# Performance work log

Hardware: AMD Instinct MI355X
Metric: run time of the kernel (lower is better)

The kernel has to match this reference:

```python
import jax, jax.numpy as jnp
import numpy as np

N, E, R, L = 20000, 160000, 3, 2
IN, HID, H, OUT = 64, 128, 16, 1
FH = HID // H   # per-head dim = 8
HD2 = HID // 2  # MLP bottleneck = 64


def setup_inputs() -> dict:
    key = jax.random.key(0)
    ks = iter(jax.random.split(key, 40))
    def w(*shape):
        return jax.random.normal(next(ks), shape, jnp.float32) * 0.05
    inp = dict(
        inputs=jax.random.normal(next(ks), (N, IN), jnp.float32),
        src=jax.random.randint(next(ks), (R, E), 0, N, dtype=jnp.int32),
        dst=jax.random.randint(next(ks), (R, E), 0, N, dtype=jnp.int32),
        e1_W=w(IN, HID), e1_b=jnp.zeros(HID), e_g=jnp.ones(HID), e_bt=jnp.zeros(HID),
        e2_W=w(HID, HID), e2_b=jnp.zeros(HID),
        gat_W=w(L, R, HID, HID), gat_al=w(L, R, H, FH), gat_ar=w(L, R, H, FH),
        gat_b=jnp.zeros((L, R, HID)),
        attn_p=w(L, R, HID),
        m1_W=w(L, HID, HD2), m1_b=jnp.zeros((L, HD2)), m_g=jnp.ones((L, HD2)), m_bt=jnp.zeros((L, HD2)),
        m2_W=w(L, HD2, HID), m2_b=jnp.zeros((L, HID)),
        d1_W=w(HID, HD2), d1_b=jnp.zeros(HD2), d_g=jnp.ones(HD2), d_bt=jnp.zeros(HD2),
        d2_W=w(HD2, OUT), d2_b=jnp.zeros(OUT),
    )
    return inp


def _bn(x, g, b):
    # BatchNorm1d, training mode: biased batch statistics, eps=1e-5
    mu = x.mean(0)
    var = jnp.mean((x - mu) ** 2, 0)
    return g * (x - mu) * jax.lax.rsqrt(var + 1e-5) + b


def _mlp(x, W1, b1, g, bt, W2, b2, skip=False):
    h = jax.nn.relu(_bn(x @ W1 + b1, g, bt))
    o = h @ W2 + b2
    return o + h if skip else o


def _gat(x, W, al, ar, b, src, dst):
    # single-relation DGL GATConv (feat_drop=attn_drop=0, neg_slope=0.2, bias)
    z = (x @ W).reshape(N, H, FH)                 # [N,H,FH]
    el = (z * al).sum(-1)                          # [N,H]
    er = (z * ar).sum(-1)                          # [N,H]
    e = jax.nn.leaky_relu(el[src] + er[dst], 0.2)  # [E,H]
    m = jax.ops.segment_max(e, dst, num_segments=N)
    m = jnp.where(jnp.isfinite(m), m, 0.0)
    ex = jnp.exp(e - m[dst])
    s = jax.ops.segment_sum(ex, dst, num_segments=N)
    alpha = ex / s[dst]                            # edge softmax over in-edges
    out = jax.ops.segment_sum(alpha[:, :, None] * z[src], dst, num_segments=N)
    return out.reshape(N, HID) + b                 # flatten heads + bias


def reference(inputs, src, dst, e1_W, e1_b, e_g, e_bt, e2_W, e2_b,
              gat_W, gat_al, gat_ar, gat_b, attn_p,
              m1_W, m1_b, m_g, m_bt, m2_W, m2_b,
              d1_W, d1_b, d_g, d_bt, d2_W, d2_b):
    h = _mlp(inputs, e1_W, e1_b, e_g, e_bt, e2_W, e2_b, skip=True)  # embed, skip
    gat_v = jax.vmap(_gat, in_axes=(None, 0, 0, 0, 0, 0, 0))        # over relations
    for l in range(L):
        stacked = gat_v(h, gat_W[l], gat_al[l], gat_ar[l], gat_b[l], src, dst)  # [R,N,HID]
        w = jax.nn.softmax(attn_p[l], axis=0)        # per-dim softmax over relations [R,HID]
        v = jnp.einsum('rnf,rf->nf', stacked, w)     # attn-weighted relation agg
        h = _mlp(v, m1_W[l], m1_b[l], m_g[l], m_bt[l], m2_W[l], m2_b[l]) + h
    return _mlp(h, d1_W, d1_b, d_g, d_bt, d2_W, d2_b)
```

## Files before the change

### kernel.cpp

```cpp
#include <hip/hip_runtime.h>
#include <math.h>

constexpr int kN   = 20000;
constexpr int kE   = 160000;
constexpr int kR   = 3;
constexpr int kL   = 2;
constexpr int kIN  = 64;
constexpr int kHID = 128;
constexpr int kH   = 16;
constexpr int kFH  = 8;
constexpr int kHD2 = 64;

typedef __bf16 bf16x8 __attribute__((ext_vector_type(8)));
typedef float  f32x4  __attribute__((ext_vector_type(4)));

__device__ __forceinline__ bf16x8 ldfrag(const __bf16* p) {
  return __builtin_bit_cast(bf16x8, *(const uint4*)p);
}
__device__ __forceinline__ f32x4 MF(bf16x8 a, bf16x8 b, f32x4 c) {
  return __builtin_amdgcn_mfma_f32_16x16x32_bf16(a, b, c, 0, 0, 0);
}

__device__ __forceinline__ void splitrow(const float* __restrict__ rowbase, int koff,
                                         bool bn, const float* scS, const float* shS,
                                         bf16x8& hi, bf16x8& lo) {
  float4 xa = *(const float4*)(rowbase + koff);
  float4 xb = *(const float4*)(rowbase + koff + 4);
  float x[8] = {xa.x, xa.y, xa.z, xa.w, xb.x, xb.y, xb.z, xb.w};
  union { __bf16 b[8]; bf16x8 v; } uh, ul;
#pragma unroll
  for (int e = 0; e < 8; e++) {
    float y = x[e];
    if (bn) y = fmaxf(fmaf(y, scS[koff + e], shS[koff + e]), 0.f);
    __bf16 hb = (__bf16)y;
    uh.b[e] = hb;
    ul.b[e] = (__bf16)(y - (float)hb);
  }
  hi = uh.v; lo = ul.v;
}

__global__ __launch_bounds__(256) void mgemm_kernel(
    const float* __restrict__ A, const __bf16* __restrict__ WT,
    const float* __restrict__ bias, const float* __restrict__ resf, int resmode,
    const float* __restrict__ bnstat, const float* __restrict__ bng,
    const float* __restrict__ bnbt, float invn,
    float* __restrict__ statS,
    float* __restrict__ Cf, __bf16* __restrict__ Chi,
    const float* __restrict__ alb, const float* __restrict__ arb,
    float* __restrict__ elout,
    int n, int k, int m, long wstride, long cstride) {
  __shared__ __bf16 Bh[64][136];
  __shared__ __bf16 Bl[64][136];
  __shared__ float scS[128], shS[128];
  const int t  = threadIdx.x;
  const int w  = t >> 6;
  const int l  = t & 63;
  const int lr = l & 15;
  const int lg = l >> 4;
  const int rb = blockIdx.x * 128 + w * 32;
  const int c0 = blockIdx.y * 64;
  const __bf16* Whi = WT + (size_t)blockIdx.z * wstride;
  const __bf16* Wlo = Whi + (size_t)k * m;
  if (Chi) Chi += (size_t)blockIdx.z * cstride;
  const float* al = alb ? alb + blockIdx.z * kHID : nullptr;
  const float* ar = arb ? arb + blockIdx.z * kHID : nullptr;
  float* elo = elout ? elout + blockIdx.z * 32 : nullptr;

  const bool bn = bnstat != nullptr;
  if (bn && t < k) {
    float mu  = bnstat[t] * invn;
    float var = bnstat[k + t] * invn - mu * mu;
    float s = bng[t] * rsqrtf(var + 1e-5f);
    scS[t] = s; shS[t] = bnbt[t] - mu * s;
  }
  const int kseg = k >> 3;
  for (int idx = t; idx < 64 * kseg; idx += 256) {
    int col = idx / kseg, seg = idx - col * kseg;
    *(uint4*)&Bh[col][seg * 8] = *(const uint4*)&Whi[(size_t)(c0 + col) * k + seg * 8];
    *(uint4*)&Bl[col][seg * 8] = *(const uint4*)&Wlo[(size_t)(c0 + col) * k + seg * 8];
  }
  __syncthreads();

  int r0 = rb + lr;      if (r0 > n - 1) r0 = n - 1;
  int r1 = rb + 16 + lr; if (r1 > n - 1) r1 = n - 1;
  f32x4 acc[2][4] = {};

  for (int ks = 0; ks < (k >> 5); ks++) {
    const int koff = ks * 32 + lg * 8;
    bf16x8 a0h, a0l, a1h, a1l;
    splitrow(&A[(size_t)r0 * k], koff, bn, scS, shS, a0h, a0l);
    splitrow(&A[(size_t)r1 * k], koff, bn, scS, shS, a1h, a1l);
#pragma unroll
    for (int j = 0; j < 4; j++) {
      bf16x8 bh = ldfrag(&Bh[j * 16 + lr][koff]);
      bf16x8 bl = ldfrag(&Bl[j * 16 + lr][koff]);
      acc[0][j] = MF(a0h, bh, acc[0][j]);
      acc[0][j] = MF(a0l, bh, acc[0][j]);
      acc[0][j] = MF(a0h, bl, acc[0][j]);
      acc[1][j] = MF(a1h, bh, acc[1][j]);
      acc[1][j] = MF(a1l, bh, acc[1][j]);
      acc[1][j] = MF(a1h, bl, acc[1][j]);
    }
  }

  float s[4] = {}, s2[4] = {};
#pragma unroll
  for (int i = 0; i < 2; i++) {
#pragma unroll
    for (int q = 0; q < 4; q++) {
      int row = rb + i * 16 + lg * 4 + q;
      bool ok = row < n;
#pragma unroll
      for (int j = 0; j < 4; j++) {
        int col = c0 + j * 16 + lr;
        float v = acc[i][j][q];
        if (bias) v += bias[col];
        size_t off = (size_t)row * m + col;
        if (ok) {
          if (resmode == 1) v += resf[off];
          else if (resmode == 2) v += fmaxf(fmaf(resf[off], scS[col], shS[col]), 0.f);
          if (Cf) Cf[off] = v;
          if (Chi) Chi[off] = (__bf16)v;
          s[j] += v; s2[j] += v * v;
        }
      }
    }
  }
  if (statS) {
    __syncthreads();
    float* red = (float*)&Bh[0][0];
#pragma unroll
    for (int j = 0; j < 4; j++) {
      float a = s[j], b = s2[j];
      a += __shfl_xor(a, 16, 64); a += __shfl_xor(a, 32, 64);
      b += __shfl_xor(b, 16, 64); b += __shfl_xor(b, 32, 64);
      if (lg == 0) { red[w * 64 + j * 16 + lr] = a; red[256 + w * 64 + j * 16 + lr] = b; }
    }
    __syncthreads();
    if (t < 64) {
      float a = red[t] + red[64 + t] + red[128 + t] + red[192 + t];
      float b = red[256 + t] + red[320 + t] + red[384 + t] + red[448 + t];
      atomicAdd(&statS[c0 + t], a);
      atomicAdd(&statS[m + c0 + t], b);
    }
  }
  if (al) {
#pragma unroll
    for (int i = 0; i < 2; i++) {
#pragma unroll
      for (int q = 0; q < 4; q++) {
        int row = rb + i * 16 + lg * 4 + q;
#pragma unroll
        for (int j = 0; j < 4; j++) {
          int col = c0 + j * 16 + lr;
          float zv = acc[i][j][q];
          float pl = zv * al[col];
          float pr = zv * ar[col];
          pl += __shfl_xor(pl, 1, 64); pl += __shfl_xor(pl, 2, 64); pl += __shfl_xor(pl, 4, 64);
          pr += __shfl_xor(pr, 1, 64); pr += __shfl_xor(pr, 2, 64); pr += __shfl_xor(pr, 4, 64);
          if ((lr & 7) == 0 && row < n) {
            int hd = col >> 3;
            elo[(size_t)row * kHID + hd * 2]     = pl;
            elo[(size_t)row * kHID + hd * 2 + 1] = pr;
          }
        }
      }
    }
  }
}

struct WDesc { const float* src; long doff; int k, m; };
struct WDescs { WDesc d[13]; };
__global__ void wprep_kernel(WDescs ds, __bf16* __restrict__ wt) {
  WDesc dd = ds.d[blockIdx.y];
  int idx = blockIdx.x * 256 + threadIdx.x;
  if (idx >= dd.k * dd.m) return;
  int row = idx / dd.m, col = idx - row * dd.m;
  float v = dd.src[idx];
  __bf16 hb = (__bf16)v;
  __bf16 lb = (__bf16)(v - (float)hb);
  wt[dd.doff + (size_t)col * dd.k + row] = hb;
  wt[dd.doff + (size_t)dd.k * dd.m + (size_t)col * dd.k + row] = lb;
}

__global__ void hist_kernel(const int* __restrict__ dst, int* __restrict__ deg) {
  int r = blockIdx.y;
  int e = blockIdx.x * 256 + threadIdx.x;
  if (e < kE) atomicAdd(&deg[r * kN + dst[r * kE + e]], 1);
}

__global__ __launch_bounds__(1024) void csr_scan_kernel(const int* __restrict__ deg,
                                                        int* __restrict__ rowptr) {
  const int r = blockIdx.y;
  const int* dg = deg + r * kN;
  int* rp = rowptr + r * (kN + 1);
  const int t = threadIdx.x;
  constexpr int C = (kN + 1023) / 1024;
  const int base = t * C;
  int sum = 0;
#pragma unroll
  for (int i = 0; i < C; i++) {
    int j = base + i;
    if (j < kN) sum += dg[j];
  }
  __shared__ int warpTot[16];
  int lane = t & 63, wid = t >> 6;
  int v = sum;
  for (int off = 1; off < 64; off <<= 1) {
    int y = __shfl_up(v, off, 64);
    if (lane >= off) v += y;
  }
  if (lane == 63) warpTot[wid] = v;
  __syncthreads();
  int wadd = 0;
#pragma unroll
  for (int i = 0; i < 16; i++) if (i < wid) wadd += warpTot[i];
  int run = wadd + v - sum;
#pragma unroll
  for (int i = 0; i < C; i++) {
    int j = base + i;
    if (j < kN) { rp[j] = run; run += dg[j]; }
  }
  if (t == 1023) rp[kN] = run;
}

__global__ void scatter_kernel(const int* __restrict__ src, const int* __restrict__ dst,
                               const int* __restrict__ rowptr, int* __restrict__ cursor,
                               int* __restrict__ col) {
  int r = blockIdx.y;
  int e = blockIdx.x * 256 + threadIdx.x;
  if (e < kE) {
    int d = dst[r * kE + e];
    int p = atomicAdd(&cursor[r * kN + d], 1);
    col[r * kE + rowptr[r * (kN + 1) + d] + p] = src[r * kE + e];
  }
}

__global__ void gat3_kernel(const int* __restrict__ rowptr, const int* __restrict__ colidx,
                            const ushort* __restrict__ z, const float* __restrict__ elr,
                            const float* __restrict__ attn_pl, const float* __restrict__ gat_bl,
                            float* __restrict__ vv) {
  __shared__ float wsmS[kR * kHID], cvecS[kHID];
  int t = threadIdx.x;
  if (t < kHID) {
    float p0 = attn_pl[t], p1 = attn_pl[kHID + t], p2 = attn_pl[2 * kHID + t];
    float mx = fmaxf(p0, fmaxf(p1, p2));
    float e0 = __expf(p0 - mx), e1 = __expf(p1 - mx), e2 = __expf(p2 - mx);
    float si = 1.f / (e0 + e1 + e2);
    wsmS[t] = e0 * si; wsmS[kHID + t] = e1 * si; wsmS[2 * kHID + t] = e2 * si;
    cvecS[t] = (e0 * gat_bl[t] + e1 * gat_bl[kHID + t] + e2 * gat_bl[2 * kHID + t]) * si;
  }
  __syncthreads();
  int idx = blockIdx.x * 256 + t;
  if (idx >= kN * kH * 2) return;
  int half = idx & 1;
  int hh   = (idx >> 1) & 15;
  int d    = idx >> 5;
  int fo   = (hh << 3) + (half << 2);
  float out[4];
#pragma unroll
  for (int f = 0; f < 4; f++) out[f] = cvecS[fo + f];
  for (int r = 0; r < kR; r++) {
    const int* rp = rowptr + r * (kN + 1);
    const int* ci = colidx + (size_t)r * kE;
    const ushort* zr = z + (size_t)r * kN * kHID;
    float erd = elr[((size_t)d << 7) + r * 32 + (hh << 1) + 1];
    int beg = rp[d], end = rp[d + 1];
    float s = 0.f;
    float acc[4] = {};
    for (int p = beg; p < end; p++) {
      int sv = ci[p];
      float v = elr[((size_t)sv << 7) + r * 32 + (hh << 1)] + erd;
      v = v > 0.f ? v : 0.2f * v;
      float ex = __expf(v);
      s += ex;
      uint2 zz = *(const uint2*)(zr + ((size_t)sv << 7) + fo);
      acc[0] = fmaf(ex, __uint_as_float(zz.x << 16),         acc[0]);
      acc[1] = fmaf(ex, __uint_as_float(zz.x & 0xffff0000u), acc[1]);
      acc[2] = fmaf(ex, __uint_as_float(zz.y << 16),         acc[2]);
      acc[3] = fmaf(ex, __uint_as_float(zz.y & 0xffff0000u), acc[3]);
    }
    float inv = s > 0.f ? 1.f / s : 0.f;
    const float* wp = wsmS + r * kHID + fo;
#pragma unroll
    for (int f = 0; f < 4; f++) out[f] = fmaf(wp[f] * inv, acc[f], out[f]);
  }
  *(float4*)(vv + ((size_t)d << 7) + fo) = make_float4(out[0], out[1], out[2], out[3]);
}

__global__ void gemv_out_kernel(const float* __restrict__ A, const float* __restrict__ statS,
                                const float* __restrict__ g, const float* __restrict__ bt,
                                float invn, const float* __restrict__ w,
                                const float* __restrict__ b, float* __restrict__ out,
                                int n, int k) {
  __shared__ float scS[kHD2], shS[kHD2];
  int t = threadIdx.x;
  if (t < k) {
    float mu  = statS[t] * invn;
    float var = statS[k + t] * invn - mu * mu;
    float s = g[t] * rsqrtf(var + 1e-5f);
    scS[t] = s; shS[t] = bt[t] - mu * s;
  }
  __syncthreads();
  int i = blockIdx.x * 256 + t;
  if (i >= n) return;
  const float4* a = (const float4*)(A + (size_t)i * k);
  float acc = b[0];
  for (int j4 = 0; j4 < k / 4; j4++) {
    float4 x = a[j4];
    int c = j4 * 4;
    acc = fmaf(fmaxf(fmaf(x.x, scS[c],     shS[c]),     0.f), w[c],     acc);
    acc = fmaf(fmaxf(fmaf(x.y, scS[c + 1], shS[c + 1]), 0.f), w[c + 1], acc);
    acc = fmaf(fmaxf(fmaf(x.z, scS[c + 2], shS[c + 2]), 0.f), w[c + 2], acc);
    acc = fmaf(fmaxf(fmaf(x.w, scS[c + 3], shS[c + 3]), 0.f), w[c + 3], acc);
  }
  out[i] = acc;
}

extern "C" void kernel_launch(void* const* d_in, const int* in_sizes, int n_in,
                              void* d_out, int out_size, void* d_ws, size_t ws_size,
                              hipStream_t stream) {
  const float* inputs = (const float*)d_in[0];
  const int*   src    = (const int*)d_in[1];
  const int*   dst    = (const int*)d_in[2];
  const float* e1_W   = (const float*)d_in[3];
  const float* e1_b   = (const float*)d_in[4];
  const float* e_g    = (const float*)d_in[5];
  const float* e_bt   = (const float*)d_in[6];
  const float* e2_W   = (const float*)d_in[7];
  const float* e2_b   = (const float*)d_in[8];
  const float* gat_W  = (const float*)d_in[9];
  const float* gat_al = (const float*)d_in[10];
  const float* gat_ar = (const float*)d_in[11];
  const float* gat_b  = (const float*)d_in[12];
  const float* attn_p = (const float*)d_in[13];
  const float* m1_W   = (const float*)d_in[14];
  const float* m1_b   = (const float*)d_in[15];
  const float* m_g    = (const float*)d_in[16];
  const float* m_bt   = (const float*)d_in[17];
  const float* m2_W   = (const float*)d_in[18];
  const float* m2_b   = (const float*)d_in[19];
  const float* d1_W   = (const float*)d_in[20];
  const float* d1_b   = (const float*)d_in[21];
  const float* d_g    = (const float*)d_in[22];
  const float* d_bt   = (const float*)d_in[23];
  const float* d2_W   = (const float*)d_in[24];
  const float* d2_b   = (const float*)d_in[25];

  float* ws = (float*)d_ws;
  size_t o = 0;
  float*  h     = ws + o; o += (size_t)kN * kHID;
  float*  bufA  = ws + o; o += (size_t)kN * kHID;
  float*  elr   = ws + o; o += (size_t)kN * kHID;
  float*  vv    = ws + o; o += (size_t)kN * kHID;
  __bf16* z     = (__bf16*)(ws + o); o += (size_t)kR * kN * kHID / 2;
  __bf16* wt    = (__bf16*)(ws + o); o += 327680 / 2;
  int* degcur   = (int*)(ws + o); o += (size_t)6 * kN;
  float* stats  = ws + o; o += 640;
  int* rowptr   = (int*)(ws + o); o += (size_t)kR * (kN + 1);
  int* colidx   = (int*)(ws + o); o += (size_t)kR * kE;
  (void)ws_size; (void)in_sizes; (void)n_in; (void)out_size;

  int* deg    = degcur;
  int* cursor = degcur + 3 * kN;
  float* stat_e1 = stats;
  float* stat_m1[2] = {stats + 256, stats + 384};
  float* stat_d1 = stats + 512;

  const long kWE1 = 0, kWE2 = 16384, kWZ = 49152;
  const long kWM1_0 = 245760, kWM1_1 = 262144, kWM2_0 = 278528, kWM2_1 = 294912, kWD1 = 311296;

  auto nb = [](long t) { return (int)((t + 255) / 256); };
  const dim3 gE(nb(kE), kR);
  const dim3 gM128((kN + 127) / 128, 2, 1);
  const dim3 gM64((kN + 127) / 128, 1, 1);
  const dim3 gMZ((kN + 127) / 128, 2, kR);
  const float invn = 1.0f / kN;
  float* F0 = nullptr; const float* cF0 = nullptr;

  hipMemsetAsync(degcur, 0, ((size_t)6 * kN + 640) * sizeof(int), stream);
  hist_kernel<<<gE, 256, 0, stream>>>(dst, deg);
  csr_scan_kernel<<<dim3(1, kR), 1024, 0, stream>>>(deg, rowptr);
  scatter_kernel<<<gE, 256, 0, stream>>>(src, dst, rowptr, cursor, colidx);

  WDescs wd;
  wd.d[0] = {e1_W, kWE1, kIN, kHID};
  wd.d[1] = {e2_W, kWE2, kHID, kHID};
  for (int i = 0; i < 6; i++) wd.d[2 + i] = {gat_W + (size_t)i * 16384, kWZ + (long)i * 32768, kHID, kHID};
  wd.d[8]  = {m1_W,        kWM1_0, kHID, kHD2};
  wd.d[9]  = {m1_W + 8192, kWM1_1, kHID, kHD2};
  wd.d[10] = {m2_W,        kWM2_0, kHD2, kHID};
  wd.d[11] = {m2_W + 8192, kWM2_1, kHD2, kHID};
  wd.d[12] = {d1_W,        kWD1,   kHID, kHD2};
  wprep_kernel<<<dim3(64, 13), 256, 0, stream>>>(wd, wt);

  mgemm_kernel<<<gM128, 256, 0, stream>>>(inputs, wt + kWE1, e1_b, cF0, 0,
                                          cF0, cF0, cF0, invn, stat_e1, bufA, nullptr,
                                          cF0, cF0, F0, kN, kIN, kHID, 0, 0);
  mgemm_kernel<<<gM128, 256, 0, stream>>>(bufA, wt + kWE2, e2_b, bufA, 2,
                                          stat_e1, e_g, e_bt, invn, F0, h, nullptr,
                                          cF0, cF0, F0, kN, kHID, kHID, 0, 0);

  for (int l = 0; l < kL; l++) {
    mgemm_kernel<<<gMZ, 256, 0, stream>>>(h, wt + kWZ + (long)l * 3 * 32768, cF0, cF0, 0,
                                          cF0, cF0, cF0, invn, F0, F0, z,
                                          gat_al + (size_t)l * kR * kHID,
                                          gat_ar + (size_t)l * kR * kHID, elr,
                                          kN, kHID, kHID, 32768, (long)kN * kHID);
    gat3_kernel<<<nb((long)kN * kH * 2), 256, 0, stream>>>(rowptr, colidx, (const ushort*)z, elr,
                                             attn_p + (size_t)l * kR * kHID,
                                             gat_b + (size_t)l * kR * kHID, vv);
    mgemm_kernel<<<gM64, 256, 0, stream>>>(vv, wt + (l ? kWM1_1 : kWM1_0),
                                           m1_b + (size_t)l * kHD2, cF0, 0,
                                           cF0, cF0, cF0, invn, stat_m1[l], bufA, nullptr,
                                           cF0, cF0, F0, kN, kHID, kHD2, 0, 0);
    mgemm_kernel<<<gM128, 256, 0, stream>>>(bufA, wt + (l ? kWM2_1 : kWM2_0),
                                            m2_b + (size_t)l * kHID, h, 1,
                                            stat_m1[l], m_g + (size_t)l * kHD2,
                                            m_bt + (size_t)l * kHD2, invn, F0, h, nullptr,
                                            cF0, cF0, F0, kN, kHD2, kHID, 0, 0);
  }

  mgemm_kernel<<<gM64, 256, 0, stream>>>(h, wt + kWD1, d1_b, cF0, 0,
                                         cF0, cF0, cF0, invn, stat_d1, bufA, nullptr,
                                         cF0, cF0, F0, kN, kHID, kHD2, 0, 0);
  gemv_out_kernel<<<nb(kN), 256, 0, stream>>>(bufA, stat_d1, d_g, d_bt, invn,
                                              d2_W, d2_b, (float*)d_out, kN, kHD2);
}
```

Baseline: 371.6 us.

## Split el/er into compact arrays and give each GAT thread a full head

Attention logits are now stored as separate compact el and er arrays (48 floats per node) instead of interleaved inside a 128-wide buffer, which shrinks the gathered footprint. The GAT aggregation kernel assigns one thread per (node, head) with 8 features loaded as a single 16-byte vector, halving the redundant logit and exp work. The edge loop is unrolled by four to keep more independent gathers in flight. The cost is half as many threads and more registers per thread, which may reduce latency hiding.

```diff
diff --git a/kernel.cpp b/kernel.cpp
--- a/kernel.cpp
+++ b/kernel.cpp
@@ -47,7 +47,7 @@
     float* __restrict__ statS,
     float* __restrict__ Cf, __bf16* __restrict__ Chi,
     const float* __restrict__ alb, const float* __restrict__ arb,
-    float* __restrict__ elout,
+    float* __restrict__ elb, float* __restrict__ erb,
     int n, int k, int m, long wstride, long cstride) {
   __shared__ __bf16 Bh[64][136];
   __shared__ __bf16 Bl[64][136];
@@ -64,7 +64,7 @@
   if (Chi) Chi += (size_t)blockIdx.z * cstride;
   const float* al = alb ? alb + blockIdx.z * kHID : nullptr;
   const float* ar = arb ? arb + blockIdx.z * kHID : nullptr;
-  float* elo = elout ? elout + blockIdx.z * 32 : nullptr;
+  if (elb) { elb += blockIdx.z * 16; erb += blockIdx.z * 16; }
 
   const bool bn = bnstat != nullptr;
   if (bn && t < k) {
@@ -160,8 +160,8 @@
           pr += __shfl_xor(pr, 1, 64); pr += __shfl_xor(pr, 2, 64); pr += __shfl_xor(pr, 4, 64);
           if ((lr & 7) == 0 && row < n) {
             int hd = col >> 3;
-            elo[(size_t)row * kHID + hd * 2]     = pl;
-            elo[(size_t)row * kHID + hd * 2 + 1] = pr;
+            elb[(size_t)row * 48 + hd] = pl;
+            erb[(size_t)row * 48 + hd] = pr;
           }
         }
       }
@@ -237,7 +237,8 @@
 }
 
 __global__ void gat3_kernel(const int* __restrict__ rowptr, const int* __restrict__ colidx,
-                            const ushort* __restrict__ z, const float* __restrict__ elr,
+                            const ushort* __restrict__ z, const float* __restrict__ elb,
+                            const float* __restrict__ erb,
                             const float* __restrict__ attn_pl, const float* __restrict__ gat_bl,
                             float* __restrict__ vv) {
   __shared__ float wsmS[kR * kHID], cvecS[kHID];
@@ -252,40 +253,74 @@
   }
   __syncthreads();
   int idx = blockIdx.x * 256 + t;
-  if (idx >= kN * kH * 2) return;
-  int half = idx & 1;
-  int hh   = (idx >> 1) & 15;
-  int d    = idx >> 5;
-  int fo   = (hh << 3) + (half << 2);
-  float out[4];
-#pragma unroll
-  for (int f = 0; f < 4; f++) out[f] = cvecS[fo + f];
+  if (idx >= kN * kH) return;
+  int d = idx >> 4, hh = idx & 15;
+  const int fo = hh << 3;
+  float out[kFH];
+#pragma unroll
+  for (int f = 0; f < kFH; f++) out[f] = cvecS[fo + f];
   for (int r = 0; r < kR; r++) {
     const int* rp = rowptr + r * (kN + 1);
     const int* ci = colidx + (size_t)r * kE;
     const ushort* zr = z + (size_t)r * kN * kHID;
-    float erd = elr[((size_t)d << 7) + r * 32 + (hh << 1) + 1];
+    const int ro = r * 16;
+    float erd = erb[(size_t)d * 48 + ro + hh];
     int beg = rp[d], end = rp[d + 1];
     float s = 0.f;
-    float acc[4] = {};
-    for (int p = beg; p < end; p++) {
+    float acc[kFH] = {};
+    int p = beg;
+    for (; p + 4 <= end; p += 4) {
+      int svA = ci[p], svB = ci[p + 1], svC = ci[p + 2], svD = ci[p + 3];
+      float vA = elb[(size_t)svA * 48 + ro + hh];
+      float vB = elb[(size_t)svB * 48 + ro + hh];
+      float vC = elb[(size_t)svC * 48 + ro + hh];
+      float vD = elb[(size_t)svD * 48 + ro + hh];
+      uint4 zA = *(const uint4*)(zr + ((size_t)svA << 7) + fo);
+      uint4 zB = *(const uint4*)(zr + ((size_t)svB << 7) + fo);
+      uint4 zC = *(const uint4*)(zr + ((size_t)svC << 7) + fo);
+      uint4 zD = *(const uint4*)(zr + ((size_t)svD << 7) + fo);
+      uint4 zz[4] = {zA, zB, zC, zD};
+      float vv4[4] = {vA, vB, vC, vD};
+#pragma unroll
+      for (int u = 0; u < 4; u++) {
+        float v = vv4[u] + erd;
+        v = v > 0.f ? v : 0.2f * v;
+        float ex = __expf(v);
+        s += ex;
+        acc[0] = fmaf(ex, __uint_as_float(zz[u].x << 16),         acc[0]);
+        acc[1] = fmaf(ex, __uint_as_float(zz[u].x & 0xffff0000u), acc[1]);
+        acc[2] = fmaf(ex, __uint_as_float(zz[u].y << 16),         acc[2]);
+        acc[3] = fmaf(ex, __uint_as_float(zz[u].y & 0xffff0000u), acc[3]);
+        acc[4] = fmaf(ex, __uint_as_float(zz[u].z << 16),         acc[4]);
+        acc[5] = fmaf(ex, __uint_as_float(zz[u].z & 0xffff0000u), acc[5]);
+        acc[6] = fmaf(ex, __uint_as_float(zz[u].w << 16),         acc[6]);
+        acc[7] = fmaf(ex, __uint_as_float(zz[u].w & 0xffff0000u), acc[7]);
+      }
+    }
+    for (; p < end; p++) {
       int sv = ci[p];
-      float v = elr[((size_t)sv << 7) + r * 32 + (hh << 1)] + erd;
+      float v = elb[(size_t)sv * 48 + ro + hh] + erd;
       v = v > 0.f ? v : 0.2f * v;
       float ex = __expf(v);
       s += ex;
-      uint2 zz = *(const uint2*)(zr + ((size_t)sv << 7) + fo);
+      uint4 zz = *(const uint4*)(zr + ((size_t)sv << 7) + fo);
       acc[0] = fmaf(ex, __uint_as_float(zz.x << 16),         acc[0]);
       acc[1] = fmaf(ex, __uint_as_float(zz.x & 0xffff0000u), acc[1]);
       acc[2] = fmaf(ex, __uint_as_float(zz.y << 16),         acc[2]);
       acc[3] = fmaf(ex, __uint_as_float(zz.y & 0xffff0000u), acc[3]);
+      acc[4] = fmaf(ex, __uint_as_float(zz.z << 16),         acc[4]);
+      acc[5] = fmaf(ex, __uint_as_float(zz.z & 0xffff0000u), acc[5]);
+      acc[6] = fmaf(ex, __uint_as_float(zz.w << 16),         acc[6]);
+      acc[7] = fmaf(ex, __uint_as_float(zz.w & 0xffff0000u), acc[7]);
     }
     float inv = s > 0.f ? 1.f / s : 0.f;
     const float* wp = wsmS + r * kHID + fo;
 #pragma unroll
-    for (int f = 0; f < 4; f++) out[f] = fmaf(wp[f] * inv, acc[f], out[f]);
-  }
-  *(float4*)(vv + ((size_t)d << 7) + fo) = make_float4(out[0], out[1], out[2], out[3]);
+    for (int f = 0; f < kFH; f++) out[f] = fmaf(wp[f] * inv, acc[f], out[f]);
+  }
+  float4* vp = (float4*)(vv + ((size_t)d << 7) + fo);
+  vp[0] = make_float4(out[0], out[1], out[2], out[3]);
+  vp[1] = make_float4(out[4], out[5], out[6], out[7]);
 }
 
 __global__ void gemv_out_kernel(const float* __restrict__ A, const float* __restrict__ statS,
@@ -351,8 +386,9 @@
   size_t o = 0;
   float*  h     = ws + o; o += (size_t)kN * kHID;
   float*  bufA  = ws + o; o += (size_t)kN * kHID;
-  float*  elr   = ws + o; o += (size_t)kN * kHID;
   float*  vv    = ws + o; o += (size_t)kN * kHID;
+  float*  elbuf = ws + o; o += (size_t)kN * 48;
+  float*  erbuf = ws + o; o += (size_t)kN * 48;
   __bf16* z     = (__bf16*)(ws + o); o += (size_t)kR * kN * kHID / 2;
   __bf16* wt    = (__bf16*)(ws + o); o += 327680 / 2;
   int* degcur   = (int*)(ws + o); o += (size_t)6 * kN;
@@ -396,34 +432,35 @@
 
   mgemm_kernel<<<gM128, 256, 0, stream>>>(inputs, wt + kWE1, e1_b, cF0, 0,
                                           cF0, cF0, cF0, invn, stat_e1, bufA, nullptr,
-                                          cF0, cF0, F0, kN, kIN, kHID, 0, 0);
+                                          cF0, cF0, F0, F0, kN, kIN, kHID, 0, 0);
   mgemm_kernel<<<gM128, 256, 0, stream>>>(bufA, wt + kWE2, e2_b, bufA, 2,
                                           stat_e1, e_g, e_bt, invn, F0, h, nullptr,
-                                          cF0, cF0, F0, kN, kHID, kHID, 0, 0);
+                                          cF0, cF0, F0, F0, kN, kHID, kHID, 0, 0);
 
   for (int l = 0; l < kL; l++) {
     mgemm_kernel<<<gMZ, 256, 0, stream>>>(h, wt + kWZ + (long)l * 3 * 32768, cF0, cF0, 0,
                                           cF0, cF0, cF0, invn, F0, F0, z,
                                           gat_al + (size_t)l * kR * kHID,
-                                          gat_ar + (size_t)l * kR * kHID, elr,
+                                          gat_ar + (size_t)l * kR * kHID, elbuf, erbuf,
                                           kN, kHID, kHID, 32768, (long)kN * kHID);
-    gat3_kernel<<<nb((long)kN * kH * 2), 256, 0, stream>>>(rowptr, colidx, (const ushort*)z, elr,
+    gat3_kernel<<<nb((long)kN * kH), 256, 0, stream>>>(rowptr, colidx, (const ushort*)z,
+                                             elbuf, erbuf,
                                              attn_p + (size_t)l * kR * kHID,
                                              gat_b + (size_t)l * kR * kHID, vv);
     mgemm_kernel<<<gM64, 256, 0, stream>>>(vv, wt + (l ? kWM1_1 : kWM1_0),
                                            m1_b + (size_t)l * kHD2, cF0, 0,
                                            cF0, cF0, cF0, invn, stat_m1[l], bufA, nullptr,
-                                           cF0, cF0, F0, kN, kHID, kHD2, 0, 0);
+                                           cF0, cF0, F0, F0, kN, kHID, kHD2, 0, 0);
     mgemm_kernel<<<gM128, 256, 0, stream>>>(bufA, wt + (l ? kWM2_1 : kWM2_0),
                                             m2_b + (size_t)l * kHID, h, 1,
                                             stat_m1[l], m_g + (size_t)l * kHD2,
                                             m_bt + (size_t)l * kHD2, invn, F0, h, nullptr,
-                                            cF0, cF0, F0, kN, kHD2, kHID, 0, 0);
+                                            cF0, cF0, F0, F0, kN, kHD2, kHID, 0, 0);
   }
 
   mgemm_kernel<<<gM64, 256, 0, stream>>>(h, wt + kWD1, d1_b, cF0, 0,
                                          cF0, cF0, cF0, invn, stat_d1, bufA, nullptr,
-                                         cF0, cF0, F0, kN, kHID, kHD2, 0, 0);
+                                         cF0, cF0, F0, F0, kN, kHID, kHD2, 0, 0);
   gemv_out_kernel<<<nb(kN), 256, 0, stream>>>(bufA, stat_d1, d_g, d_bt, invn,
                                               d2_W, d2_b, (float*)d_out, kN, kHD2);
 }
```

Result: faster. 342.8 us (-7.7%).
